# Performance work log

Measured on AMD Instinct MI355X. Metric: run time of the kernel, lower is better.

The kernel has to match this reference:

```python
import jax, jax.numpy as jnp
import numpy as np

N, E, F_IN, H, D, HID, G = 50000, 800000, 64, 4, 32, 128, 1024
NEG_SLOPE = 0.2


def setup_inputs():
    key = jax.random.key(0)
    ks = jax.random.split(key, 32)
    inp = {
        "x": jax.random.normal(ks[0], (N, F_IN), dtype=jnp.float32),
        "edge_index": jax.random.randint(ks[1], (2, E), 0, N, dtype=jnp.int64),
        "batch": jnp.sort(jax.random.randint(ks[2], (N,), 0, G, dtype=jnp.int64)),
    }
    dims = [F_IN, HID, HID]
    i = 3
    for l, din in enumerate(dims):
        s = 1.0 / np.sqrt(din)
        inp[f"Wl{l}"] = jax.random.normal(ks[i], (din, H * D), dtype=jnp.float32) * s; i += 1
        inp[f"bl{l}"] = jnp.zeros((H * D,), dtype=jnp.float32)
        inp[f"Wr{l}"] = jax.random.normal(ks[i], (din, H * D), dtype=jnp.float32) * s; i += 1
        inp[f"br{l}"] = jnp.zeros((H * D,), dtype=jnp.float32)
        inp[f"att{l}"] = jax.random.normal(ks[i], (H, D), dtype=jnp.float32) * (1.0 / np.sqrt(D)); i += 1
        inp[f"b{l}"] = jnp.zeros((H * D,), dtype=jnp.float32)
    inp["Wh"] = jax.random.normal(ks[i], (HID, 1), dtype=jnp.float32) * (1.0 / np.sqrt(HID))
    inp["bh"] = jnp.zeros((1,), dtype=jnp.float32)
    return inp


def gatv2_layer(x, src, dst, Wl, bl, Wr, br, att, b):
    # GATv2Conv (eval mode, no dropout): e_ij = att . leaky_relu(Wl x_j + Wr x_i)
    xl = (x @ Wl + bl).reshape(-1, H, D)   # source transform
    xr = (x @ Wr + br).reshape(-1, H, D)   # target transform
    m = xl[src] + xr[dst]                  # [E,H,D]
    e = jnp.where(m >= 0, m, NEG_SLOPE * m)
    score = jnp.einsum("ehd,hd->eh", e, att)          # [E,H]
    smax = jax.ops.segment_max(score, dst, num_segments=N)  # [N,H]
    expv = jnp.exp(score - smax[dst])
    denom = jax.ops.segment_sum(expv, dst, num_segments=N)
    alpha = expv / denom[dst]                          # softmax over in-edges of dst
    agg = jax.ops.segment_sum(alpha[:, :, None] * xl[src], dst, num_segments=N)
    return agg.reshape(-1, H * D) + b


def reference(x, edge_index, batch, Wl0, bl0, Wr0, br0, att0, b0,
              Wl1, bl1, Wr1, br1, att1, b1,
              Wl2, bl2, Wr2, br2, att2, b2, Wh, bh):
    src, dst = edge_index[0], edge_index[1]
    params = [(Wl0, bl0, Wr0, br0, att0, b0),
              (Wl1, bl1, Wr1, br1, att1, b1),
              (Wl2, bl2, Wr2, br2, att2, b2)]
    h = x
    for p in params:
        h = gatv2_layer(h, src, dst, *p)
        h = jax.nn.elu(h)  # dropout inactive in eval
    # global mean pool over graphs
    sums = jax.ops.segment_sum(h, batch, num_segments=G)
    cnt = jax.ops.segment_sum(jnp.ones((h.shape[0],), h.dtype), batch, num_segments=G)
    pooled = sums / jnp.maximum(cnt, 1.0)[:, None]
    return pooled @ Wh + bh
```

## Files before the change

### kernel.cpp

```cpp
#include <hip/hip_runtime.h>
#include <math.h>

#define N_NODES 50000
#define N_EDGES 800000
#define HD 128
#define GG 1024
#define NEG_SLOPE 0.2f
#define SCAN_B 1024
#define NB ((N_NODES + SCAN_B - 1) / SCAN_B)

typedef __attribute__((ext_vector_type(8))) short bf16x8;
typedef __attribute__((ext_vector_type(4))) float f32x4;

__device__ __forceinline__ unsigned short f2bf(float v) {
    unsigned u = __float_as_uint(v);
    u += 0x7fff + ((u >> 16) & 1);
    return (unsigned short)(u >> 16);
}
__device__ __forceinline__ float bf2f(unsigned short s) {
    return __uint_as_float((unsigned)s << 16);
}

__global__ void convert_x(const float* __restrict__ x, unsigned short* __restrict__ Xh,
                          unsigned short* __restrict__ Xl, int total)
{
    int i = blockIdx.x * 256 + threadIdx.x;
    if (i >= total) return;
    float v = x[i];
    unsigned short hi = f2bf(v);
    unsigned short lo = f2bf(v - bf2f(hi));
    Xh[i] = hi; Xl[i] = lo;
}

__global__ void convert_w(const float* __restrict__ Wl, const float* __restrict__ Wr,
                          unsigned short* __restrict__ Wth, unsigned short* __restrict__ Wtl,
                          int K)
{
    int t = blockIdx.x * 256 + threadIdx.x;
    if (t >= 256 * K) return;
    int c = t / K, k = t - c * K;
    float v = (c < 128) ? Wl[(size_t)k * 128 + c] : Wr[(size_t)k * 128 + (c - 128)];
    unsigned short hi = f2bf(v);
    unsigned short lo = f2bf(v - bf2f(hi));
    Wth[t] = hi; Wtl[t] = lo;
}

template<int K>
__launch_bounds__(256)
__global__ void gemm_mfma(const unsigned short* __restrict__ Xh, const unsigned short* __restrict__ Xl,
                          const unsigned short* __restrict__ Wth, const unsigned short* __restrict__ Wtl,
                          const float* __restrict__ bl, const float* __restrict__ br,
                          float* __restrict__ Cl, float* __restrict__ Cr, int n)
{
    constexpr int KC = 32;
    constexpr int NCH = K / KC;
    constexpr int XR = 40;
    __shared__ unsigned short XsH[64 * XR], XsL[64 * XR];
    __shared__ unsigned short WsH[256 * XR], WsL[256 * XR];
    const int tid  = threadIdx.x;
    const int wave = tid >> 6;
    const int lane = tid & 63;
    const int quad = lane >> 4;
    const int l15  = lane & 15;
    const int row0 = blockIdx.x * 64;

    f32x4 acc[4][4];
    #pragma unroll
    for (int i = 0; i < 4; i++)
        #pragma unroll
        for (int j = 0; j < 4; j++) acc[i][j] = (f32x4){0.f, 0.f, 0.f, 0.f};

    for (int ch = 0; ch < NCH; ch++) {
        const int k0 = ch * KC;
        {
            const int r = tid >> 2, seg = tid & 3;
            const int row = row0 + r;
            const size_t go = (size_t)row * K + k0 + seg * 8;
            uint4 vh = make_uint4(0, 0, 0, 0), vl = make_uint4(0, 0, 0, 0);
            if (row < n) { vh = *(const uint4*)(Xh + go); vl = *(const uint4*)(Xl + go); }
            *(uint4*)&XsH[r * XR + seg * 8] = vh;
            *(uint4*)&XsL[r * XR + seg * 8] = vl;
        }
        #pragma unroll
        for (int i = 0; i < 4; i++) {
            const int f = tid + i * 256;
            const int wr = f >> 2, seg = f & 3;
            const size_t go = (size_t)wr * K + k0 + seg * 8;
            *(uint4*)&WsH[wr * XR + seg * 8] = *(const uint4*)(Wth + go);
            *(uint4*)&WsL[wr * XR + seg * 8] = *(const uint4*)(Wtl + go);
        }
        __syncthreads();

        bf16x8 ah[4], al[4];
        #pragma unroll
        for (int mt = 0; mt < 4; mt++) {
            ah[mt] = *(const bf16x8*)&XsH[(mt * 16 + l15) * XR + quad * 8];
            al[mt] = *(const bf16x8*)&XsL[(mt * 16 + l15) * XR + quad * 8];
        }
        #pragma unroll
        for (int nt = 0; nt < 4; nt++) {
            const int wr = wave * 64 + nt * 16 + l15;
            const bf16x8 bh = *(const bf16x8*)&WsH[wr * XR + quad * 8];
            const bf16x8 bo = *(const bf16x8*)&WsL[wr * XR + quad * 8];
            #pragma unroll
            for (int mt = 0; mt < 4; mt++) {
                acc[mt][nt] = __builtin_amdgcn_mfma_f32_16x16x32_bf16(ah[mt], bh, acc[mt][nt], 0, 0, 0);
                acc[mt][nt] = __builtin_amdgcn_mfma_f32_16x16x32_bf16(ah[mt], bo, acc[mt][nt], 0, 0, 0);
                acc[mt][nt] = __builtin_amdgcn_mfma_f32_16x16x32_bf16(al[mt], bh, acc[mt][nt], 0, 0, 0);
            }
        }
        __syncthreads();
    }

    const bool isL = (wave < 2);
    const int colbase = (wave & 1) * 64;
    const float* bias = isL ? bl : br;
    float* C = isL ? Cl : Cr;
    #pragma unroll
    for (int nt = 0; nt < 4; nt++) {
        const float bv = bias[colbase + nt * 16 + l15];
        #pragma unroll
        for (int mt = 0; mt < 4; mt++) {
            #pragma unroll
            for (int r = 0; r < 4; r++) {
                const int row = row0 + mt * 16 + quad * 4 + r;
                if (row < n)
                    C[(size_t)row * 128 + colbase + nt * 16 + l15] = acc[mt][nt][r] + bv;
            }
        }
    }
}

__global__ void deg_hist(const int* __restrict__ dst, int* __restrict__ deg) {
    int e = blockIdx.x * 256 + threadIdx.x;
    if (e < N_EDGES) atomicAdd(&deg[dst[e]], 1);
}

__launch_bounds__(SCAN_B)
__global__ void scan_block(const int* __restrict__ deg, int* __restrict__ rowptr,
                           int* __restrict__ btot)
{
    __shared__ int s[SCAN_B];
    const int tid = threadIdx.x;
    const int i = blockIdx.x * SCAN_B + tid;
    int v = (i < N_NODES) ? deg[i] : 0;
    s[tid] = v;
    __syncthreads();
    for (int off = 1; off < SCAN_B; off <<= 1) {
        int t = (tid >= off) ? s[tid - off] : 0;
        __syncthreads();
        s[tid] += t;
        __syncthreads();
    }
    if (i < N_NODES) rowptr[i] = s[tid] - v;
    if (tid == SCAN_B - 1) btot[blockIdx.x] = s[SCAN_B - 1];
}

__global__ void scan_btot(const int* __restrict__ btot, int* __restrict__ boff) {
    if (threadIdx.x == 0) {
        int a = 0;
        for (int b = 0; b < NB; b++) { boff[b] = a; a += btot[b]; }
        boff[NB] = a;
    }
}

__global__ void scan_add(const int* __restrict__ boff, int* __restrict__ rowptr,
                         int* __restrict__ cursor)
{
    int i = blockIdx.x * 256 + threadIdx.x;
    if (i < N_NODES) {
        int r = rowptr[i] + boff[i >> 10];
        rowptr[i] = r;
        cursor[i] = r;
    }
    if (i == N_NODES) rowptr[N_NODES] = boff[NB];
}

__global__ void scatter_csr(const int* __restrict__ src, const int* __restrict__ dst,
                            int* __restrict__ cursor, int* __restrict__ csr_src)
{
    int e = blockIdx.x * 256 + threadIdx.x;
    if (e >= N_EDGES) return;
    int pos = atomicAdd(&cursor[dst[e]], 1);
    csr_src[pos] = src[e];
}

__global__ void build_gptr(const int* __restrict__ batch, int* __restrict__ gptr) {
    int i = blockIdx.x * 256 + threadIdx.x;
    if (i > N_NODES) return;
    if (i == 0) {
        for (int g = 0; g <= batch[0]; g++) gptr[g] = 0;
    } else if (i == N_NODES) {
        for (int g = batch[N_NODES - 1] + 1; g <= GG; g++) gptr[g] = N_NODES;
    } else {
        int b0 = batch[i - 1], b1 = batch[i];
        for (int g = b0 + 1; g <= b1; g++) gptr[g] = i;
    }
}

__launch_bounds__(256)
__global__ void node_attn(const float* __restrict__ xl, const float* __restrict__ xr,
                          const int* __restrict__ rowptr, const int* __restrict__ csr_src,
                          const float* __restrict__ att, const float* __restrict__ bvec,
                          unsigned short* __restrict__ Hh, unsigned short* __restrict__ Hl)
{
    const int node = (blockIdx.x * 256 + threadIdx.x) >> 6;
    const int lane = threadIdx.x & 63;
    if (node >= N_NODES) return;
    const int half = lane >> 5;
    const int li   = lane & 31;

    const float4 xrd = *(const float4*)(xr + (size_t)node * HD + li * 4);
    const float4 aw  = *(const float4*)(att + li * 4);
    const int beg = rowptr[node];
    const int end = rowptr[node + 1];

    float m = -1e30f, l = 0.f;
    float4 acc = make_float4(0.f, 0.f, 0.f, 0.f);

    int e0 = beg + half;
    int s0 = (e0 < end) ? csr_src[e0] : 0;
    float4 v = *(const float4*)(xl + (size_t)s0 * HD + li * 4);

    for (int base = beg; base < end; base += 2) {
        const bool valid = (base + half) < end;
        float4 vn = v;
        if (base + 2 < end) {
            int e2 = base + 2 + half;
            int s2 = (e2 < end) ? csr_src[e2] : 0;
            vn = *(const float4*)(xl + (size_t)s2 * HD + li * 4);
        }
        float t0 = v.x + xrd.x; t0 = (t0 >= 0.f) ? t0 : NEG_SLOPE * t0;
        float t1 = v.y + xrd.y; t1 = (t1 >= 0.f) ? t1 : NEG_SLOPE * t1;
        float t2 = v.z + xrd.z; t2 = (t2 >= 0.f) ? t2 : NEG_SLOPE * t2;
        float t3 = v.w + xrd.w; t3 = (t3 >= 0.f) ? t3 : NEG_SLOPE * t3;
        float p = t0 * aw.x + t1 * aw.y + t2 * aw.z + t3 * aw.w;
        p += __shfl_xor(p, 1);
        p += __shfl_xor(p, 2);
        p += __shfl_xor(p, 4);
        const float mn = valid ? fmaxf(m, p) : m;
        const float w  = valid ? __expf(p - mn) : 0.f;
        const float sc = __expf(m - mn);
        l = l * sc + w;
        acc.x = acc.x * sc + w * v.x;
        acc.y = acc.y * sc + w * v.y;
        acc.z = acc.z * sc + w * v.z;
        acc.w = acc.w * sc + w * v.w;
        m = mn;
        v = vn;
    }

    const float mo = __shfl_xor(m, 32);
    const float lo = __shfl_xor(l, 32);
    float4 ao;
    ao.x = __shfl_xor(acc.x, 32);
    ao.y = __shfl_xor(acc.y, 32);
    ao.z = __shfl_xor(acc.z, 32);
    ao.w = __shfl_xor(acc.w, 32);
    const float mm = fmaxf(m, mo);
    const float e1 = __expf(m - mm);
    const float e2 = __expf(mo - mm);
    const float ll = l * e1 + lo * e2;
    const float inv = (ll > 0.f) ? 1.f / ll : 0.f;
    const float4 bb = *(const float4*)(bvec + li * 4);
    float o0 = (acc.x * e1 + ao.x * e2) * inv + bb.x;
    float o1 = (acc.y * e1 + ao.y * e2) * inv + bb.y;
    float o2 = (acc.z * e1 + ao.z * e2) * inv + bb.z;
    float o3 = (acc.w * e1 + ao.w * e2) * inv + bb.w;
    o0 = (o0 > 0.f) ? o0 : expm1f(o0);
    o1 = (o1 > 0.f) ? o1 : expm1f(o1);
    o2 = (o2 > 0.f) ? o2 : expm1f(o2);
    o3 = (o3 > 0.f) ? o3 : expm1f(o3);
    if (half == 0) {
        unsigned short h0 = f2bf(o0), h1 = f2bf(o1), h2 = f2bf(o2), h3 = f2bf(o3);
        unsigned short l0 = f2bf(o0 - bf2f(h0)), l1 = f2bf(o1 - bf2f(h1));
        unsigned short l2 = f2bf(o2 - bf2f(h2)), l3 = f2bf(o3 - bf2f(h3));
        *(ushort4*)(Hh + (size_t)node * HD + li * 4) = make_ushort4(h0, h1, h2, h3);
        *(ushort4*)(Hl + (size_t)node * HD + li * 4) = make_ushort4(l0, l1, l2, l3);
    }
}

__launch_bounds__(256)
__global__ void pool_head(const unsigned short* __restrict__ Hh, const unsigned short* __restrict__ Hl,
                          const int* __restrict__ gptr, const float* __restrict__ Wh,
                          const float* __restrict__ bh, float* __restrict__ out)
{
    const int g = (blockIdx.x * 256 + threadIdx.x) >> 6;
    const int lane = threadIdx.x & 63;
    if (g >= GG) return;
    const int b0 = gptr[g], b1 = gptr[g + 1];
    const float2 w = *(const float2*)(Wh + lane * 2);
    float sx = 0.f, sy = 0.f;
    for (int i = b0; i < b1; i++) {
        const unsigned vh = *(const unsigned*)(Hh + (size_t)i * HD + lane * 2);
        const unsigned vl = *(const unsigned*)(Hl + (size_t)i * HD + lane * 2);
        sx += bf2f((unsigned short)(vh & 0xffff)) + bf2f((unsigned short)(vl & 0xffff));
        sy += bf2f((unsigned short)(vh >> 16))    + bf2f((unsigned short)(vl >> 16));
    }
    float d = sx * w.x + sy * w.y;
    d += __shfl_xor(d, 1);
    d += __shfl_xor(d, 2);
    d += __shfl_xor(d, 4);
    d += __shfl_xor(d, 8);
    d += __shfl_xor(d, 16);
    d += __shfl_xor(d, 32);
    if (lane == 0) out[g] = d / fmaxf((float)(b1 - b0), 1.f) + bh[0];
}

extern "C" void kernel_launch(void* const* d_in, const int* in_sizes, int n_in,
                              void* d_out, int out_size, void* d_ws, size_t ws_size,
                              hipStream_t stream)
{
    const float* x     = (const float*)d_in[0];
    const int*   edge  = (const int*)d_in[1];
    const int*   batch = (const int*)d_in[2];
    const int*   src   = edge;
    const int*   dst   = edge + N_EDGES;
    const float* Wh    = (const float*)d_in[21];
    const float* bh    = (const float*)d_in[22];
    float* out = (float*)d_out;

    const size_t N128 = (size_t)N_NODES * HD;
    float* buf_xl = (float*)d_ws;
    float* buf_xr = buf_xl + N128;
    unsigned short* Xh  = (unsigned short*)(buf_xr + N128);
    unsigned short* Xl_ = Xh + N128;
    unsigned short* Wth = Xl_ + N128;
    unsigned short* Wtl = Wth + 3 * 256 * 128;
    int* deg     = (int*)(Wtl + 3 * 256 * 128);
    int* rowptr  = deg + N_NODES;
    int* cursor  = rowptr + N_NODES + 1;
    int* csr_src = cursor + N_NODES;
    int* btot    = csr_src + N_EDGES;
    int* boff    = btot + NB;
    int* gptr    = boff + NB + 1;

    hipMemsetAsync(deg, 0, (size_t)N_NODES * sizeof(int), stream);
    deg_hist<<<(N_EDGES + 255) / 256, 256, 0, stream>>>(dst, deg);
    scan_block<<<NB, SCAN_B, 0, stream>>>(deg, rowptr, btot);
    scan_btot<<<1, 64, 0, stream>>>(btot, boff);
    scan_add<<<(N_NODES + 256) / 256, 256, 0, stream>>>(boff, rowptr, cursor);
    scatter_csr<<<(N_EDGES + 255) / 256, 256, 0, stream>>>(src, dst, cursor, csr_src);
    build_gptr<<<(N_NODES + 256) / 256, 256, 0, stream>>>(batch, gptr);

    convert_x<<<(N_NODES * 64 + 255) / 256, 256, 0, stream>>>(x, Xh, Xl_, N_NODES * 64);
    for (int l = 0; l < 3; l++) {
        const int K = (l == 0) ? 64 : 128;
        convert_w<<<(256 * K + 255) / 256, 256, 0, stream>>>(
            (const float*)d_in[3 + 6 * l], (const float*)d_in[5 + 6 * l],
            Wth + l * 256 * 128, Wtl + l * 256 * 128, K);
    }

    const int gemm_grid = (N_NODES + 63) / 64;
    const int attn_grid = (N_NODES + 3) / 4;

    for (int l = 0; l < 3; l++) {
        const float* bl  = (const float*)d_in[4 + 6 * l];
        const float* br  = (const float*)d_in[6 + 6 * l];
        const float* att = (const float*)d_in[7 + 6 * l];
        const float* bb  = (const float*)d_in[8 + 6 * l];

        if (l == 0)
            gemm_mfma<64><<<gemm_grid, 256, 0, stream>>>(Xh, Xl_, Wth, Wtl,
                                                         bl, br, buf_xl, buf_xr, N_NODES);
        else
            gemm_mfma<128><<<gemm_grid, 256, 0, stream>>>(Xh, Xl_,
                                                          Wth + l * 256 * 128, Wtl + l * 256 * 128,
                                                          bl, br, buf_xl, buf_xr, N_NODES);
        node_attn<<<attn_grid, 256, 0, stream>>>(buf_xl, buf_xr, rowptr, csr_src,
                                                 att, bb, Xh, Xl_);
    }

    pool_head<<<GG / 4, 256, 0, stream>>>(Xh, Xl_, gptr, Wh, bh, out);
}
```

Measured before the change: 517.3 us.

## Process four edges per wavefront in GATv2 attention with 16-lane groups

The per-node attention kernel now splits each 64-lane wavefront into four 16-lane groups, each handling one edge with 8 channels per lane, instead of two 32-lane halves with 4 channels each. This halves loop trips for the average degree-16 node and gives more gather loads in flight per iteration. The online-softmax partial states of the four groups are merged with a two-step butterfly shuffle, and the output uses 16-byte bf16x8 stores. Register pressure rises with doubled accumulators, and nodes with few in-edges leave more groups idle.

```diff
diff --git a/kernel.cpp b/kernel.cpp
--- a/kernel.cpp
+++ b/kernel.cpp
@@ -207,76 +207,110 @@
     const int node = (blockIdx.x * 256 + threadIdx.x) >> 6;
     const int lane = threadIdx.x & 63;
     if (node >= N_NODES) return;
-    const int half = lane >> 5;
-    const int li   = lane & 31;
-
-    const float4 xrd = *(const float4*)(xr + (size_t)node * HD + li * 4);
-    const float4 aw  = *(const float4*)(att + li * 4);
+    const int grp = lane >> 4;
+    const int li  = lane & 15;
+
+    const size_t nb = (size_t)node * HD + li * 8;
+    const float4 xr0 = *(const float4*)(xr + nb);
+    const float4 xr1 = *(const float4*)(xr + nb + 4);
+    const float4 aw0 = *(const float4*)(att + li * 8);
+    const float4 aw1 = *(const float4*)(att + li * 8 + 4);
     const int beg = rowptr[node];
     const int end = rowptr[node + 1];
 
     float m = -1e30f, l = 0.f;
-    float4 acc = make_float4(0.f, 0.f, 0.f, 0.f);
-
-    int e0 = beg + half;
+    float4 a0 = make_float4(0.f, 0.f, 0.f, 0.f);
+    float4 a1 = make_float4(0.f, 0.f, 0.f, 0.f);
+
+    int e0 = beg + grp;
     int s0 = (e0 < end) ? csr_src[e0] : 0;
-    float4 v = *(const float4*)(xl + (size_t)s0 * HD + li * 4);
-
-    for (int base = beg; base < end; base += 2) {
-        const bool valid = (base + half) < end;
-        float4 vn = v;
-        if (base + 2 < end) {
-            int e2 = base + 2 + half;
-            int s2 = (e2 < end) ? csr_src[e2] : 0;
-            vn = *(const float4*)(xl + (size_t)s2 * HD + li * 4);
-        }
-        float t0 = v.x + xrd.x; t0 = (t0 >= 0.f) ? t0 : NEG_SLOPE * t0;
-        float t1 = v.y + xrd.y; t1 = (t1 >= 0.f) ? t1 : NEG_SLOPE * t1;
-        float t2 = v.z + xrd.z; t2 = (t2 >= 0.f) ? t2 : NEG_SLOPE * t2;
-        float t3 = v.w + xrd.w; t3 = (t3 >= 0.f) ? t3 : NEG_SLOPE * t3;
-        float p = t0 * aw.x + t1 * aw.y + t2 * aw.z + t3 * aw.w;
+    float4 v0 = *(const float4*)(xl + (size_t)s0 * HD + li * 8);
+    float4 v1 = *(const float4*)(xl + (size_t)s0 * HD + li * 8 + 4);
+
+    for (int base = beg; base < end; base += 4) {
+        const bool valid = (base + grp) < end;
+        float4 n0 = v0, n1 = v1;
+        if (base + 4 < end) {
+            const int e2 = base + 4 + grp;
+            const int s2 = (e2 < end) ? csr_src[e2] : 0;
+            n0 = *(const float4*)(xl + (size_t)s2 * HD + li * 8);
+            n1 = *(const float4*)(xl + (size_t)s2 * HD + li * 8 + 4);
+        }
+        float t, p;
+        t = v0.x + xr0.x; t = fmaxf(t, NEG_SLOPE * t); p  = t * aw0.x;
+        t = v0.y + xr0.y; t = fmaxf(t, NEG_SLOPE * t); p  = fmaf(t, aw0.y, p);
+        t = v0.z + xr0.z; t = fmaxf(t, NEG_SLOPE * t); p  = fmaf(t, aw0.z, p);
+        t = v0.w + xr0.w; t = fmaxf(t, NEG_SLOPE * t); p  = fmaf(t, aw0.w, p);
+        t = v1.x + xr1.x; t = fmaxf(t, NEG_SLOPE * t); p  = fmaf(t, aw1.x, p);
+        t = v1.y + xr1.y; t = fmaxf(t, NEG_SLOPE * t); p  = fmaf(t, aw1.y, p);
+        t = v1.z + xr1.z; t = fmaxf(t, NEG_SLOPE * t); p  = fmaf(t, aw1.z, p);
+        t = v1.w + xr1.w; t = fmaxf(t, NEG_SLOPE * t); p  = fmaf(t, aw1.w, p);
         p += __shfl_xor(p, 1);
         p += __shfl_xor(p, 2);
-        p += __shfl_xor(p, 4);
+
         const float mn = valid ? fmaxf(m, p) : m;
         const float w  = valid ? __expf(p - mn) : 0.f;
         const float sc = __expf(m - mn);
-        l = l * sc + w;
-        acc.x = acc.x * sc + w * v.x;
-        acc.y = acc.y * sc + w * v.y;
-        acc.z = acc.z * sc + w * v.z;
-        acc.w = acc.w * sc + w * v.w;
+        l = fmaf(l, sc, w);
+        a0.x = fmaf(a0.x, sc, w * v0.x);
+        a0.y = fmaf(a0.y, sc, w * v0.y);
+        a0.z = fmaf(a0.z, sc, w * v0.z);
+        a0.w = fmaf(a0.w, sc, w * v0.w);
+        a1.x = fmaf(a1.x, sc, w * v1.x);
+        a1.y = fmaf(a1.y, sc, w * v1.y);
+        a1.z = fmaf(a1.z, sc, w * v1.z);
+        a1.w = fmaf(a1.w, sc, w * v1.w);
         m = mn;
-        v = vn;
-    }
-
-    const float mo = __shfl_xor(m, 32);
-    const float lo = __shfl_xor(l, 32);
-    float4 ao;
-    ao.x = __shfl_xor(acc.x, 32);
-    ao.y = __shfl_xor(acc.y, 32);
-    ao.z = __shfl_xor(acc.z, 32);
-    ao.w = __shfl_xor(acc.w, 32);
-    const float mm = fmaxf(m, mo);
-    const float e1 = __expf(m - mm);
-    const float e2 = __expf(mo - mm);
-    const float ll = l * e1 + lo * e2;
-    const float inv = (ll > 0.f) ? 1.f / ll : 0.f;
-    const float4 bb = *(const float4*)(bvec + li * 4);
-    float o0 = (acc.x * e1 + ao.x * e2) * inv + bb.x;
-    float o1 = (acc.y * e1 + ao.y * e2) * inv + bb.y;
-    float o2 = (acc.z * e1 + ao.z * e2) * inv + bb.z;
-    float o3 = (acc.w * e1 + ao.w * e2) * inv + bb.w;
-    o0 = (o0 > 0.f) ? o0 : expm1f(o0);
-    o1 = (o1 > 0.f) ? o1 : expm1f(o1);
-    o2 = (o2 > 0.f) ? o2 : expm1f(o2);
-    o3 = (o3 > 0.f) ? o3 : expm1f(o3);
-    if (half == 0) {
-        unsigned short h0 = f2bf(o0), h1 = f2bf(o1), h2 = f2bf(o2), h3 = f2bf(o3);
-        unsigned short l0 = f2bf(o0 - bf2f(h0)), l1 = f2bf(o1 - bf2f(h1));
-        unsigned short l2 = f2bf(o2 - bf2f(h2)), l3 = f2bf(o3 - bf2f(h3));
-        *(ushort4*)(Hh + (size_t)node * HD + li * 4) = make_ushort4(h0, h1, h2, h3);
-        *(ushort4*)(Hl + (size_t)node * HD + li * 4) = make_ushort4(l0, l1, l2, l3);
+        v0 = n0; v1 = n1;
+    }
+
+    #pragma unroll
+    for (int off = 16; off < 64; off <<= 1) {
+        const float mo = __shfl_xor(m, off);
+        const float lo = __shfl_xor(l, off);
+        float4 b0, b1;
+        b0.x = __shfl_xor(a0.x, off); b0.y = __shfl_xor(a0.y, off);
+        b0.z = __shfl_xor(a0.z, off); b0.w = __shfl_xor(a0.w, off);
+        b1.x = __shfl_xor(a1.x, off); b1.y = __shfl_xor(a1.y, off);
+        b1.z = __shfl_xor(a1.z, off); b1.w = __shfl_xor(a1.w, off);
+        const float mm = fmaxf(m, mo);
+        const float e1 = __expf(m - mm);
+        const float e2 = __expf(mo - mm);
+        l = l * e1 + lo * e2;
+        a0.x = a0.x * e1 + b0.x * e2;
+        a0.y = a0.y * e1 + b0.y * e2;
+        a0.z = a0.z * e1 + b0.z * e2;
+        a0.w = a0.w * e1 + b0.w * e2;
+        a1.x = a1.x * e1 + b1.x * e2;
+        a1.y = a1.y * e1 + b1.y * e2;
+        a1.z = a1.z * e1 + b1.z * e2;
+        a1.w = a1.w * e1 + b1.w * e2;
+        m = mm;
+    }
+
+    if (grp == 0) {
+        const float inv = (l > 0.f) ? 1.f / l : 0.f;
+        const float4 bb0 = *(const float4*)(bvec + li * 8);
+        const float4 bb1 = *(const float4*)(bvec + li * 8 + 4);
+        float o[8];
+        o[0] = fmaf(a0.x, inv, bb0.x);
+        o[1] = fmaf(a0.y, inv, bb0.y);
+        o[2] = fmaf(a0.z, inv, bb0.z);
+        o[3] = fmaf(a0.w, inv, bb0.w);
+        o[4] = fmaf(a1.x, inv, bb1.x);
+        o[5] = fmaf(a1.y, inv, bb1.y);
+        o[6] = fmaf(a1.z, inv, bb1.z);
+        o[7] = fmaf(a1.w, inv, bb1.w);
+        bf16x8 hv, lv;
+        #pragma unroll
+        for (int j = 0; j < 8; j++) {
+            float e = (o[j] > 0.f) ? o[j] : expm1f(o[j]);
+            unsigned short h = f2bf(e);
+            hv[j] = (short)h;
+            lv[j] = (short)f2bf(e - bf2f(h));
+        }
+        *(bf16x8*)(Hh + nb) = hv;
+        *(bf16x8*)(Hl + nb) = lv;
     }
 }
 
```

Result: no change. 516.2 us (-0.2%).
